# Performance work log

Hardware: AMD Instinct MI355X
Metric: run time of the kernel (lower is better)

## Reference

```python
import jax, jax.numpy as jnp
import numpy as np

BSZ, SEQ, HID = 4, 4096, 2048
NUM_EXPERTS, TOPK = 64, 8


def setup_inputs() -> dict:
    key = jax.random.key(0)
    kx, kw = jax.random.split(key)
    x = jax.random.normal(kx, (BSZ, SEQ, HID), dtype=jnp.float32)
    # nn.Linear default init scale ~ 1/sqrt(fan_in); exact init irrelevant for correctness baseline
    W = jax.random.normal(kw, (NUM_EXPERTS, HID), dtype=jnp.float32) * (HID ** -0.5)
    b = jnp.zeros((NUM_EXPERTS,), dtype=jnp.float32)
    return {"x": x, "W": W, "b": b}


def reference(x, W, b):
    # gate: (bsz, seq, num_experts)
    gate = jnp.einsum("bsh,eh->bse", x, W) + b
    # top-k along expert dim
    logits, ids = jax.lax.top_k(gate, TOPK)  # (bsz, seq, topk)
    # scatter top-k logits into a -inf mask, then softmax over all experts
    bsz, seq, ne = gate.shape
    bi = jnp.arange(bsz)[:, None, None]
    si = jnp.arange(seq)[None, :, None]
    mask = jnp.full(gate.shape, -jnp.inf, dtype=gate.dtype)
    mask = mask.at[bi, si, ids].set(logits)
    probs = jax.nn.softmax(mask, axis=-1)  # zeros outside top-k
    return (probs, ids)
```

## Files before the change

### kernel.cpp

```cpp
#include <hip/hip_runtime.h>
#include <math.h>

#define BSZ 4
#define SEQ 4096
#define HID 2048
#define NE 64
#define TOPK 8
#define NTOK (BSZ*SEQ)
#define NSPLIT 4
#define KSPL (HID/NSPLIT)
#define KC 64
#define BT 64

#define XS 68
#define WSS 68

__global__ __launch_bounds__(256, 4)
void moe_gate_gemm(const float* __restrict__ x, const float* __restrict__ W,
                   float* __restrict__ part) {
    __shared__ __align__(16) float xlds[KC * XS];
    __shared__ __align__(16) float wlds[KC * WSS];

    const int tid   = threadIdx.x;
    const int tile  = blockIdx.x;
    const int split = blockIdx.y;
    const int T0 = tile * BT;
    const int k0 = split * KSPL;

    const int tx = tid & 15;
    const int ty = tid >> 4;

    const int row = tid & 63;
    const int q   = tid >> 6;

    double acc[4][4];
    #pragma unroll
    for (int i = 0; i < 4; i++)
        #pragma unroll
        for (int j = 0; j < 4; j++) acc[i][j] = 0.0;

    for (int c = 0; c < KSPL / KC; c++) {
        const int kc = k0 + c * KC;

        #pragma unroll
        for (int r = 0; r < 4; r++) {
            const int k4 = r * 4 + q;
            const float4 xv = *reinterpret_cast<const float4*>(
                &x[(size_t)(T0 + row) * HID + kc + k4 * 4]);
            xlds[(k4 * 4 + 0) * XS + row] = xv.x;
            xlds[(k4 * 4 + 1) * XS + row] = xv.y;
            xlds[(k4 * 4 + 2) * XS + row] = xv.z;
            xlds[(k4 * 4 + 3) * XS + row] = xv.w;
            const float4 wv = *reinterpret_cast<const float4*>(
                &W[(size_t)row * HID + kc + k4 * 4]);
            wlds[(k4 * 4 + 0) * WSS + row] = wv.x;
            wlds[(k4 * 4 + 1) * WSS + row] = wv.y;
            wlds[(k4 * 4 + 2) * WSS + row] = wv.z;
            wlds[(k4 * 4 + 3) * WSS + row] = wv.w;
        }
        __syncthreads();

        #pragma unroll 4
        for (int k = 0; k < KC; k++) {
            const float4 xv = *reinterpret_cast<const float4*>(&xlds[k * XS + ty * 4]);
            const float4 wv = *reinterpret_cast<const float4*>(&wlds[k * WSS + tx * 4]);
            const float xr[4] = {xv.x, xv.y, xv.z, xv.w};
            const float wr[4] = {wv.x, wv.y, wv.z, wv.w};
            #pragma unroll
            for (int i = 0; i < 4; i++)
                #pragma unroll
                for (int j = 0; j < 4; j++)
                    acc[i][j] += (double)xr[i] * (double)wr[j];
        }
        __syncthreads();
    }

    #pragma unroll
    for (int i = 0; i < 4; i++) {
        const int tok = T0 + ty * 4 + i;
        const float4 v = make_float4((float)acc[i][0], (float)acc[i][1],
                                     (float)acc[i][2], (float)acc[i][3]);
        *reinterpret_cast<float4*>(
            &part[((size_t)split * NTOK + tok) * NE + tx * 4]) = v;
    }
}

__global__ __launch_bounds__(256)
void moe_topk_softmax(const float* __restrict__ part, const float* __restrict__ b,
                      float* __restrict__ probs, float* __restrict__ ids) {
    const int lane  = threadIdx.x & 63;
    const int w     = threadIdx.x >> 6;
    const int token = blockIdx.x * 4 + w;

    float g = b[lane];
    #pragma unroll
    for (int s = 0; s < NSPLIT; s++)
        g += part[((size_t)s * NTOK + token) * NE + lane];

    const float gorig = g;
    float cur = g;
    float m = 0.f, denom = 0.f;
    int   myid = 0;
    bool  sel = false;

    #pragma unroll
    for (int it = 0; it < TOPK; it++) {
        float v = cur;
        int idx = lane;
        #pragma unroll
        for (int d = 1; d < 64; d <<= 1) {
            const float ov = __shfl_xor(v, d, 64);
            const int   oi = __shfl_xor(idx, d, 64);
            if (ov > v || (ov == v && oi < idx)) { v = ov; idx = oi; }
        }
        if (it == 0) m = v;
        denom += expf(v - m);
        if (lane == idx) { sel = true; cur = -INFINITY; }
        if (lane == it)  myid = idx;
    }

    probs[(size_t)token * NE + lane] = sel ? expf(gorig - m) / denom : 0.f;
    if (lane < TOPK) ids[(size_t)token * TOPK + lane] = (float)myid;
}

extern "C" void kernel_launch(void* const* d_in, const int* in_sizes, int n_in,
                              void* d_out, int out_size, void* d_ws, size_t ws_size,
                              hipStream_t stream) {
    const float* x = (const float*)d_in[0];
    const float* W = (const float*)d_in[1];
    const float* b = (const float*)d_in[2];

    float* probs = (float*)d_out;
    float* ids   = (float*)d_out + (size_t)NTOK * NE;
    float* part  = (float*)d_ws;

    dim3 g1(NTOK / BT, NSPLIT);
    moe_gate_gemm<<<g1, 256, 0, stream>>>(x, W, part);
    moe_topk_softmax<<<NTOK / 4, 256, 0, stream>>>(part, b, probs, ids);
}
```

Before: 280.1 us.

## Use FP64 MFMA for gate GEMM with register-prefetched global loads

```diff
diff --git a/kernel.cpp b/kernel.cpp
--- a/kernel.cpp
+++ b/kernel.cpp
@@ -12,14 +12,16 @@
 #define KC 64
 #define BT 64
 
-#define XS 68
-#define WSS 68
+#define XS 72
+#define WSS 72
+
+typedef double f64x4 __attribute__((ext_vector_type(4)));
 
 __global__ __launch_bounds__(256, 4)
 void moe_gate_gemm(const float* __restrict__ x, const float* __restrict__ W,
                    float* __restrict__ part) {
-    __shared__ __align__(16) float xlds[KC * XS];
-    __shared__ __align__(16) float wlds[KC * WSS];
+    __shared__ float xlds[KC * XS];
+    __shared__ float wlds[KC * WSS];
 
     const int tid   = threadIdx.x;
     const int tile  = blockIdx.x;
@@ -27,61 +29,86 @@
     const int T0 = tile * BT;
     const int k0 = split * KSPL;
 
-    const int tx = tid & 15;
-    const int ty = tid >> 4;
+    const int wv   = tid >> 6;
+    const int lane = tid & 63;
+    const int kof  = lane >> 4;
+    const int col  = lane & 15;
 
-    const int row = tid & 63;
-    const int q   = tid >> 6;
+    const int srow = tid & 63;
 
-    double acc[4][4];
+    const double a1 = (kof == 0) ? (double)col : 0.0;
+    const double b1 = (kof == 0) ? 1.0 : 0.0;
+    const double a2 = (kof == 0) ? 1.0 : 0.0;
+    const double b2 = (kof == 0) ? (double)col : 0.0;
+    const f64x4 zero = (f64x4){0.0, 0.0, 0.0, 0.0};
+    const f64x4 cal1 = __builtin_amdgcn_mfma_f64_16x16x4f64(a1, b1, zero, 0, 0, 0);
+    const f64x4 cal2 = __builtin_amdgcn_mfma_f64_16x16x4f64(a2, b2, zero, 0, 0, 0);
+    int drow[4], dcol[4];
     #pragma unroll
-    for (int i = 0; i < 4; i++)
-        #pragma unroll
-        for (int j = 0; j < 4; j++) acc[i][j] = 0.0;
+    for (int a = 0; a < 4; a++) {
+        drow[a] = (int)cal1[a];
+        dcol[a] = (int)cal2[a];
+    }
+
+    f64x4 acc[4];
+    #pragma unroll
+    for (int nt = 0; nt < 4; nt++) acc[nt] = zero;
+
+    const int base_a = kof * XS  + wv * 16 + col;
+    const int base_b = kof * WSS + col;
+
+    float4 px[4], pw[4];
+    #pragma unroll
+    for (int r = 0; r < 4; r++) {
+        const int k4 = wv * 4 + r;
+        px[r] = *reinterpret_cast<const float4*>(&x[(size_t)(T0 + srow) * HID + k0 + k4 * 4]);
+        pw[r] = *reinterpret_cast<const float4*>(&W[(size_t)srow  * HID + k0 + k4 * 4]);
+    }
 
     for (int c = 0; c < KSPL / KC; c++) {
-        const int kc = k0 + c * KC;
-
+        __syncthreads();
         #pragma unroll
         for (int r = 0; r < 4; r++) {
-            const int k4 = r * 4 + q;
-            const float4 xv = *reinterpret_cast<const float4*>(
-                &x[(size_t)(T0 + row) * HID + kc + k4 * 4]);
-            xlds[(k4 * 4 + 0) * XS + row] = xv.x;
-            xlds[(k4 * 4 + 1) * XS + row] = xv.y;
-            xlds[(k4 * 4 + 2) * XS + row] = xv.z;
-            xlds[(k4 * 4 + 3) * XS + row] = xv.w;
-            const float4 wv = *reinterpret_cast<const float4*>(
-                &W[(size_t)row * HID + kc + k4 * 4]);
-            wlds[(k4 * 4 + 0) * WSS + row] = wv.x;
-            wlds[(k4 * 4 + 1) * WSS + row] = wv.y;
-            wlds[(k4 * 4 + 2) * WSS + row] = wv.z;
-            wlds[(k4 * 4 + 3) * WSS + row] = wv.w;
+            const int k4 = wv * 4 + r;
+            xlds[(k4 * 4 + 0) * XS + srow] = px[r].x;
+            xlds[(k4 * 4 + 1) * XS + srow] = px[r].y;
+            xlds[(k4 * 4 + 2) * XS + srow] = px[r].z;
+            xlds[(k4 * 4 + 3) * XS + srow] = px[r].w;
+            wlds[(k4 * 4 + 0) * WSS + srow] = pw[r].x;
+            wlds[(k4 * 4 + 1) * WSS + srow] = pw[r].y;
+            wlds[(k4 * 4 + 2) * WSS + srow] = pw[r].z;
+            wlds[(k4 * 4 + 3) * WSS + srow] = pw[r].w;
+        }
+        if (c + 1 < KSPL / KC) {
+            const int kc = k0 + (c + 1) * KC;
+            #pragma unroll
+            for (int r = 0; r < 4; r++) {
+                const int k4 = wv * 4 + r;
+                px[r] = *reinterpret_cast<const float4*>(&x[(size_t)(T0 + srow) * HID + kc + k4 * 4]);
+                pw[r] = *reinterpret_cast<const float4*>(&W[(size_t)srow  * HID + kc + k4 * 4]);
+            }
         }
         __syncthreads();
 
-        #pragma unroll 4
-        for (int k = 0; k < KC; k++) {
-            const float4 xv = *reinterpret_cast<const float4*>(&xlds[k * XS + ty * 4]);
-            const float4 wv = *reinterpret_cast<const float4*>(&wlds[k * WSS + tx * 4]);
-            const float xr[4] = {xv.x, xv.y, xv.z, xv.w};
-            const float wr[4] = {wv.x, wv.y, wv.z, wv.w};
+        #pragma unroll
+        for (int kb = 0; kb < KC / 4; kb++) {
+            const double ad = (double)xlds[kb * (4 * XS) + base_a];
             #pragma unroll
-            for (int i = 0; i < 4; i++)
-                #pragma unroll
-                for (int j = 0; j < 4; j++)
-                    acc[i][j] += (double)xr[i] * (double)wr[j];
+            for (int nt = 0; nt < 4; nt++) {
+                const double bd = (double)wlds[kb * (4 * WSS) + base_b + nt * 16];
+                acc[nt] = __builtin_amdgcn_mfma_f64_16x16x4f64(ad, bd, acc[nt], 0, 0, 0);
+            }
         }
-        __syncthreads();
     }
 
     #pragma unroll
-    for (int i = 0; i < 4; i++) {
-        const int tok = T0 + ty * 4 + i;
-        const float4 v = make_float4((float)acc[i][0], (float)acc[i][1],
-                                     (float)acc[i][2], (float)acc[i][3]);
-        *reinterpret_cast<float4*>(
-            &part[((size_t)split * NTOK + tok) * NE + tx * 4]) = v;
+    for (int nt = 0; nt < 4; nt++) {
+        #pragma unroll
+        for (int a = 0; a < 4; a++) {
+            const int tok = T0 + wv * 16 + drow[a];
+            const int e   = nt * 16 + dcol[a];
+            part[((size_t)split * NTOK + tok) * NE + e] = (float)acc[nt][a];
+        }
     }
 }
 
```

Result: faster. 249.4 us (-11.0%).
